# Kernel optimization log

Hardware: AMD Instinct MI355X
Metric: run time of the kernel (lower is better)

## Reference

```python
import jax, jax.numpy as jnp
import numpy as np
import math

B, S, D, H = 4, 1024, 512, 8
DK = D // H
NEG = -1e32


def setup_inputs() -> dict:
    key = jax.random.key(0)
    ks = jax.random.split(key, 16)
    f = lambda k, shape: jax.random.normal(k, shape, dtype=jnp.float32)
    w = 1.0 / math.sqrt(D)  # xavier-ish scale
    return {
        'query_mean': f(ks[0], (B, S, D)),
        'query_cov': f(ks[1], (B, S, D)),
        'key_mean': f(ks[2], (B, S, D)),
        'key_cov': f(ks[3], (B, S, D)),
        'values_mean': f(ks[4], (B, S, D)),
        'values_cov': f(ks[5], (B, S, D)),
        'Wk_mean': f(ks[6], (D, D)) * w, 'bk_mean': jnp.zeros((D,), jnp.float32),
        'Wk_cov': f(ks[7], (D, D)) * w, 'bk_cov': jnp.zeros((D,), jnp.float32),
        'Wv_mean': f(ks[8], (D, D)) * w, 'bv_mean': jnp.zeros((D,), jnp.float32),
        'Wv_cov': f(ks[9], (D, D)) * w, 'bv_cov': jnp.zeros((D,), jnp.float32),
        'Wo_mean': f(ks[10], (D, D)) * w, 'bo_mean': jnp.zeros((D,), jnp.float32),
        'Wo_cov': f(ks[11], (D, D)) * w, 'bo_cov': jnp.zeros((D,), jnp.float32),
        'gammas': f(ks[12], (H, 1, 1)) * 0.1,
        'mask': jnp.tril(jnp.ones((1, 1, S, S), dtype=jnp.int32)),
    }


def _forward(query_mean, query_cov, key_mean, key_cov, values_mean, values_cov,
             Wk_mean, bk_mean, Wk_cov, bk_cov, Wv_mean, bv_mean, Wv_cov, bv_cov,
             Wo_mean, bo_mean, Wo_cov, bo_cov, gammas, mask):
    def heads(x, W, b):  # [B,S,D] -> [B,H,S,DK]
        return (x @ W + b).reshape(B, S, H, DK).transpose(0, 2, 1, 3)

    # kq_same=True: queries and keys share the k linears
    qm = heads(query_mean, Wk_mean, bk_mean)
    qc = heads(query_cov, Wk_cov, bk_cov)
    km = heads(key_mean, Wk_mean, bk_mean)
    kc = heads(key_cov, Wk_cov, bk_cov)
    vm = heads(values_mean, Wv_mean, bv_mean)
    vc = heads(values_cov, Wv_cov, bv_cov)

    inv = 1.0 / math.sqrt(DK)
    sm = jnp.einsum('bhqd,bhkd->bhqk', qm, km) * inv  # [B,H,S,S]
    sc = jnp.einsum('bhqd,bhkd->bhqk', qc, kc) * inv

    maskf = mask.astype(jnp.float32)
    # position_effect[i,j] = |j - i|
    pos = jnp.abs(jnp.arange(S)[None, :] - jnp.arange(S)[:, None]).astype(jnp.float32)[None, None]

    def dist_scores(s):
        p = jax.nn.softmax(jnp.where(mask == 0, NEG, s), axis=-1) * maskf
        cum = jnp.cumsum(p, axis=-1)
        tot = jnp.sum(p, axis=-1, keepdims=True)
        return jnp.sqrt(jnp.clip((tot - cum) * pos, 0.0, None))

    dm = jax.lax.stop_gradient(dist_scores(sm))  # torch no_grad + detach
    dc = jax.lax.stop_gradient(dist_scores(sc))

    gv = -jax.nn.softplus(gammas)[None]  # [1,H,1,1]
    em = jnp.clip(jnp.exp(dm * gv), 1e-5, 1e5)
    ec = jnp.clip(jnp.exp(dc * gv), 1e-5, 1e5)

    am = jax.nn.softmax(jnp.where(mask == 0, NEG, sm * em), axis=-1)
    ac = jax.nn.softmax(jnp.where(mask == 0, NEG, sc * ec), axis=-1)

    om = jnp.einsum('bhqk,bhkd->bhqd', am, vm).transpose(0, 2, 1, 3).reshape(B, S, D)
    oc = jnp.einsum('bhqk,bhkd->bhqd', ac, vc).transpose(0, 2, 1, 3).reshape(B, S, D)
    return om @ Wo_mean + bo_mean, oc @ Wo_cov + bo_cov


def reference(query_mean, query_cov, key_mean, key_cov, values_mean, values_cov,
              Wk_mean, bk_mean, Wk_cov, bk_cov, Wv_mean, bv_mean, Wv_cov, bv_cov,
              Wo_mean, bo_mean, Wo_cov, bo_cov, gammas, mask):
    return _forward(query_mean, query_cov, key_mean, key_cov, values_mean, values_cov,
                    Wk_mean, bk_mean, Wk_cov, bk_cov, Wv_mean, bv_mean, Wv_cov, bv_cov,
                    Wo_mean, bo_mean, Wo_cov, bo_cov, gammas, mask)
```

## Files before the change

kernel.cpp:

```cpp
#include <hip/hip_runtime.h>
#include <hip/hip_bf16.h>
#include <math.h>

constexpr int B_  = 4;
constexpr int S_  = 1024;
constexpr int D_  = 512;
constexpr int H_  = 8;
constexpr int DK_ = 64;
constexpr int MROWS_ = B_ * S_;
constexpr size_t SZ_ = (size_t)B_ * H_ * S_ * DK_;
constexpr size_t WSZ_ = (size_t)D_ * D_;

typedef __attribute__((ext_vector_type(8))) short bf16x8;
typedef __attribute__((ext_vector_type(4))) float f32x4;

__device__ __forceinline__ float bf2f(unsigned short u) {
  union { unsigned int u; float f; } v; v.u = (unsigned int)u << 16; return v.f;
}
__device__ __forceinline__ unsigned short f2bf(float f) {
  union { float f; unsigned int u; } v; v.f = f;
  unsigned int r = v.u + 0x7FFFu + ((v.u >> 16) & 1u);
  return (unsigned short)(r >> 16);
}
__device__ __forceinline__ unsigned short f2bf_ru(float f) {
  union { float f; unsigned int u; } v; v.f = f;
  return (unsigned short)((v.u + 0x8000u) >> 16);
}

__device__ __forceinline__ float ex2(float x) {
#if __has_builtin(__builtin_amdgcn_exp2f)
  return __builtin_amdgcn_exp2f(x);
#else
  float r; asm("v_exp_f32 %0, %1" : "=v"(r) : "v"(x)); return r;
#endif
}
__device__ __forceinline__ float fsqrt_raw(float x) {
#if __has_builtin(__builtin_amdgcn_sqrtf)
  return __builtin_amdgcn_sqrtf(x);
#else
  float r; asm("v_sqrt_f32 %0, %1" : "=v"(r) : "v"(x)); return r;
#endif
}
__device__ __forceinline__ float frcp_raw(float x) {
#if __has_builtin(__builtin_amdgcn_rcpf)
  return __builtin_amdgcn_rcpf(x);
#else
  float r; asm("v_rcp_f32 %0, %1" : "=v"(r) : "v"(x)); return r;
#endif
}

template <int CTRL>
__device__ __forceinline__ float dpp_mov_f(float x) {
  return __builtin_bit_cast(float,
      __builtin_amdgcn_update_dpp(0, __builtin_bit_cast(int, x), CTRL, 0xF, 0xF, true));
}
__device__ __forceinline__ float scan16(float v) {
  v += dpp_mov_f<0x111>(v);
  v += dpp_mov_f<0x112>(v);
  v += dpp_mov_f<0x114>(v);
  v += dpp_mov_f<0x118>(v);
  return v;
}
__device__ __forceinline__ float red16(float v) {
  v += dpp_mov_f<0x128>(v);
  v += dpp_mov_f<0x124>(v);
  v += dpp_mov_f<0x122>(v);
  v += dpp_mov_f<0x121>(v);
  return v;
}
__device__ __forceinline__ float bcast15(float v) {
  return __builtin_bit_cast(float,
      __builtin_amdgcn_ds_swizzle(__builtin_bit_cast(int, v), 0x01F0));
}

__device__ __forceinline__ void gll16(const unsigned short* g, unsigned short* l) {
  __builtin_amdgcn_global_load_lds(
      (const __attribute__((address_space(1))) unsigned int*)g,
      (__attribute__((address_space(3))) unsigned int*)l, 16, 0, 0);
}

struct CvtArgs { const float* src[6]; unsigned short* dst; };

__global__ __launch_bounds__(256) void a2bf(CvtArgs a) {
  const int z = blockIdx.z;
  const float* __restrict__ src = a.src[z];
  unsigned short* __restrict__ dst = a.dst + (size_t)z * MROWS_ * D_;
  const int idx = blockIdx.x * 256 + threadIdx.x;
#pragma unroll
  for (int i = 0; i < 8; ++i) {
    const size_t j = (size_t)idx + (size_t)i * 65536;
    const float4 v = *(const float4*)&src[j * 4];
    ushort4 p;
    p.x = f2bf(v.x); p.y = f2bf(v.y); p.z = f2bf(v.z); p.w = f2bf(v.w);
    *(ushort4*)&dst[j * 4] = p;
  }
}

struct TpArgs { const float* W[6]; unsigned short* out[6]; };

__global__ __launch_bounds__(256) void wtrans(TpArgs a) {
  const int z = blockIdx.z;
  const float* __restrict__ W = a.W[z];
  unsigned short* __restrict__ out = a.out[z];
  __shared__ float T[64][65];
  const int tid = threadIdx.x;
  const int tx = blockIdx.x & 7, ty = blockIdx.x >> 3;
  const int k0 = ty * 64, n0 = tx * 64;
#pragma unroll
  for (int i = 0; i < 4; ++i) {
    const int idx = tid + i * 256;
    const int r = idx >> 4, c4 = (idx & 15) * 4;
    const float4 w = *(const float4*)&W[(size_t)(k0 + r) * D_ + n0 + c4];
    T[r][c4 + 0] = w.x; T[r][c4 + 1] = w.y; T[r][c4 + 2] = w.z; T[r][c4 + 3] = w.w;
  }
  __syncthreads();
#pragma unroll
  for (int i = 0; i < 4; ++i) {
    const int idx = tid + i * 256;
    const int n = idx >> 4, kc = (idx & 15) * 4;
    ushort4 pk;
    pk.x = f2bf(T[kc + 0][n]); pk.y = f2bf(T[kc + 1][n]);
    pk.z = f2bf(T[kc + 2][n]); pk.w = f2bf(T[kc + 3][n]);
    *(ushort4*)&out[(size_t)(n0 + n) * D_ + k0 + kc] = pk;
  }
}

struct ProjArgs {
  const unsigned short* A[6]; const unsigned short* Wt[6]; const float* bias[6];
  unsigned short* out[6]; int vmode[6];
};

__global__ __launch_bounds__(256) void proj_mfma(ProjArgs args) {
  const int z = blockIdx.z;
  const unsigned short* __restrict__ A = args.A[z];
  const unsigned short* __restrict__ Wt = args.Wt[z];
  const float* __restrict__ bias = args.bias[z];
  unsigned short* __restrict__ out = args.out[z];
  const int vmode = args.vmode[z];

  __shared__ unsigned short Abuf[128][32];
  __shared__ unsigned short Bbuf[128][32];
  const int tid = threadIdx.x, wv = tid >> 6, lane = tid & 63;
  const int quad = lane >> 4, l16 = lane & 15;
  const int wm = wv >> 1, wn = wv & 1;
  const int n0 = blockIdx.x * 128, m0 = blockIdx.y * 128;

  f32x4 acc[4][4];
#pragma unroll
  for (int i = 0; i < 4; ++i)
#pragma unroll
    for (int j = 0; j < 4; ++j) acc[i][j] = (f32x4){0.f, 0.f, 0.f, 0.f};

  for (int kt = 0; kt < 16; ++kt) {
    const int k0 = kt * 32;
    __syncthreads();
#pragma unroll
    for (int i = 0; i < 2; ++i) {
      const int idx = tid + i * 256;
      const int m = idx >> 2, c = idx & 3;
      gll16(&A[(size_t)(m0 + m) * D_ + k0 + c * 8], &Abuf[m][c * 8]);
    }
#pragma unroll
    for (int i = 0; i < 2; ++i) {
      const int idx = tid + i * 256;
      const int n = idx >> 2, c = idx & 3;
      gll16(&Wt[(size_t)(n0 + n) * D_ + k0 + c * 8], &Bbuf[n][c * 8]);
    }
    __syncthreads();

    bf16x8 af[4], bfr[4];
#pragma unroll
    for (int i = 0; i < 4; ++i) af[i] = *(const bf16x8*)&Abuf[wm * 64 + i * 16 + l16][quad * 8];
#pragma unroll
    for (int j = 0; j < 4; ++j) bfr[j] = *(const bf16x8*)&Bbuf[wn * 64 + j * 16 + l16][quad * 8];
#pragma unroll
    for (int i = 0; i < 4; ++i)
#pragma unroll
      for (int j = 0; j < 4; ++j)
        acc[i][j] = __builtin_amdgcn_mfma_f32_16x16x32_bf16(af[i], bfr[j], acc[i][j], 0, 0, 0);
  }

#pragma unroll
  for (int j = 0; j < 4; ++j) {
    const int col = n0 + wn * 64 + j * 16 + l16;
    const float bv = bias[col];
    const int h = col >> 6, dk = col & 63;
#pragma unroll
    for (int i = 0; i < 4; ++i) {
      const int mbase = m0 + wm * 64 + i * 16 + quad * 4;
      const int b = mbase >> 10;
      if (!vmode) {
#pragma unroll
        for (int r = 0; r < 4; ++r) {
          const int s = (mbase + r) & 1023;
          out[(((size_t)b * H_ + h) * S_ + s) * DK_ + dk] = f2bf(acc[i][j][r] + bv);
        }
      } else {
        const int s = mbase & 1023;
        ushort4 pk;
        pk.x = f2bf(acc[i][j][0] + bv); pk.y = f2bf(acc[i][j][1] + bv);
        pk.z = f2bf(acc[i][j][2] + bv); pk.w = f2bf(acc[i][j][3] + bv);
        *(ushort4*)&out[(((size_t)b * H_ + h) * DK_ + dk) * S_ + s] = pk;
      }
    }
  }
}

struct OutArgs {
  const unsigned short* A[2]; const unsigned short* Wt[2];
  const float* bias[2]; float* out[2];
};

__global__ __launch_bounds__(256) void out_mfma(OutArgs args) {
  const int z = blockIdx.z;
  const unsigned short* __restrict__ A = args.A[z];
  const unsigned short* __restrict__ Wt = args.Wt[z];
  const float* __restrict__ bias = args.bias[z];
  float* __restrict__ out = args.out[z];

  __shared__ unsigned short Abuf[128][32];
  __shared__ unsigned short Bbuf[128][32];
  const int tid = threadIdx.x, wv = tid >> 6, lane = tid & 63;
  const int quad = lane >> 4, l16 = lane & 15;
  const int wm = wv >> 1, wn = wv & 1;
  const int n0 = blockIdx.x * 128, m0 = blockIdx.y * 128;

  f32x4 acc[4][4];
#pragma unroll
  for (int i = 0; i < 4; ++i)
#pragma unroll
    for (int j = 0; j < 4; ++j) acc[i][j] = (f32x4){0.f, 0.f, 0.f, 0.f};

  for (int kt = 0; kt < 16; ++kt) {
    const int k0 = kt * 32;
    __syncthreads();
#pragma unroll
    for (int i = 0; i < 2; ++i) {
      const int idx = tid + i * 256;
      const int m = idx >> 2, c = idx & 3;
      gll16(&A[(size_t)(m0 + m) * D_ + k0 + c * 8], &Abuf[m][c * 8]);
    }
#pragma unroll
    for (int i = 0; i < 2; ++i) {
      const int idx = tid + i * 256;
      const int n = idx >> 2, c = idx & 3;
      gll16(&Wt[(size_t)(n0 + n) * D_ + k0 + c * 8], &Bbuf[n][c * 8]);
    }
    __syncthreads();

    bf16x8 af[4], bfr[4];
#pragma unroll
    for (int i = 0; i < 4; ++i) af[i] = *(const bf16x8*)&Abuf[wm * 64 + i * 16 + l16][quad * 8];
#pragma unroll
    for (int j = 0; j < 4; ++j) bfr[j] = *(const bf16x8*)&Bbuf[wn * 64 + j * 16 + l16][quad * 8];
#pragma unroll
    for (int i = 0; i < 4; ++i)
#pragma unroll
      for (int j = 0; j < 4; ++j)
        acc[i][j] = __builtin_amdgcn_mfma_f32_16x16x32_bf16(af[i], bfr[j], acc[i][j], 0, 0, 0);
  }

#pragma unroll
  for (int j = 0; j < 4; ++j) {
    const int col = n0 + wn * 64 + j * 16 + l16;
    const float bv = bias[col];
#pragma unroll
    for (int i = 0; i < 4; ++i) {
      const int mbase = m0 + wm * 64 + i * 16 + quad * 4;
#pragma unroll
      for (int r = 0; r < 4; ++r)
        out[(size_t)(mbase + r) * D_ + col] = acc[i][j][r] + bv;
    }
  }
}

__global__ __launch_bounds__(512) void attn_mfma(
    const unsigned short* __restrict__ qkv, const float* __restrict__ gammas,
    unsigned short* __restrict__ Obase)
{
  __shared__ unsigned short Ps[8][16][72];

  const int tid = threadIdx.x;
  const int w = tid >> 6, lane = tid & 63, quad = lane >> 4, l16 = lane & 15;
  const int bh = blockIdx.x;
  const int pair = blockIdx.y;
  const int ch = blockIdx.z;
  const int qt = (w < 4) ? (15 - pair) : pair;
  const int wq = w & 3;
  const int q0 = qt << 6;
  const int b = bh >> 3, h = bh & 7;

  constexpr float SC_ = 0.125f * 1.4426950408889634f;
  constexpr float LOG2E_ = 1.4426950408889634f;

  const unsigned short* Q  = qkv + (size_t)ch * 3 * SZ_ + (size_t)bh * S_ * DK_;
  const unsigned short* K  = qkv + (size_t)ch * 3 * SZ_ + SZ_ + (size_t)bh * S_ * DK_;
  const unsigned short* Vt = qkv + (size_t)ch * 3 * SZ_ + 2 * SZ_ + (size_t)bh * (size_t)DK_ * S_;
  unsigned short* O = Obase + (size_t)ch * SZ_;

  const float g = gammas[h];
  const float gv2 = -(fmaxf(g, 0.f) + log1pf(__expf(-fabsf(g)))) * LOG2E_;

  const unsigned short* Qrow = Q + (size_t)(q0 + wq * 16 + l16) * DK_;
  const bf16x8 qf0 = *(const bf16x8*)(Qrow + quad * 8);
  const bf16x8 qf1 = *(const bf16x8*)(Qrow + 32 + quad * 8);
  const int myrow = q0 + wq * 16 + quad * 4;

  float Tacc[4] = {0.f, 0.f, 0.f, 0.f};
  for (int kt = 0; kt <= qt; ++kt) {
    f32x4 sa[4];
#pragma unroll
    for (int cb = 0; cb < 4; ++cb) {
      const unsigned short* Kr = K + (size_t)(kt * 64 + cb * 16 + l16) * DK_;
      const bf16x8 kf0 = *(const bf16x8*)(Kr + quad * 8);
      const bf16x8 kf1 = *(const bf16x8*)(Kr + 32 + quad * 8);
      f32x4 a = {0.f, 0.f, 0.f, 0.f};
      a = __builtin_amdgcn_mfma_f32_16x16x32_bf16(qf0, kf0, a, 0, 0, 0);
      a = __builtin_amdgcn_mfma_f32_16x16x32_bf16(qf1, kf1, a, 0, 0, 0);
      sa[cb] = a;
    }
    if (kt == qt) {
#pragma unroll
      for (int cb = 0; cb < 4; ++cb)
#pragma unroll
        for (int r = 0; r < 4; ++r) {
          float e = ex2(sa[cb][r] * SC_);
          if ((kt * 64 + cb * 16 + l16) > (myrow + r)) e = 0.f;
          Tacc[r] += e;
        }
    } else {
#pragma unroll
      for (int cb = 0; cb < 4; ++cb)
#pragma unroll
        for (int r = 0; r < 4; ++r)
          Tacc[r] += ex2(sa[cb][r] * SC_);
    }
  }
  float invT[4];
#pragma unroll
  for (int r = 0; r < 4; ++r) invT[r] = frcp_raw(red16(Tacc[r]));

  float carry[4] = {0.f, 0.f, 0.f, 0.f};
  float l2a[4] = {0.f, 0.f, 0.f, 0.f};
  f32x4 oacc[4];
#pragma unroll
  for (int cb = 0; cb < 4; ++cb) oacc[cb] = (f32x4){0.f, 0.f, 0.f, 0.f};

  for (int kt = 0; kt <= qt; ++kt) {
    bf16x8 vf0[4], vf1[4];
#pragma unroll
    for (int cb = 0; cb < 4; ++cb) {
      const unsigned short* Vr = Vt + (size_t)(cb * 16 + l16) * S_ + kt * 64;
      vf0[cb] = *(const bf16x8*)(Vr + quad * 8);
      vf1[cb] = *(const bf16x8*)(Vr + 32 + quad * 8);
    }

    f32x4 sa[4];
#pragma unroll
    for (int cb = 0; cb < 4; ++cb) {
      const unsigned short* Kr = K + (size_t)(kt * 64 + cb * 16 + l16) * DK_;
      const bf16x8 kf0 = *(const bf16x8*)(Kr + quad * 8);
      const bf16x8 kf1 = *(const bf16x8*)(Kr + 32 + quad * 8);
      f32x4 a = {0.f, 0.f, 0.f, 0.f};
      a = __builtin_amdgcn_mfma_f32_16x16x32_bf16(qf0, kf0, a, 0, 0, 0);
      a = __builtin_amdgcn_mfma_f32_16x16x32_bf16(qf1, kf1, a, 0, 0, 0);
      sa[cb] = a;
    }
#pragma unroll
    for (int cb = 0; cb < 4; ++cb)
#pragma unroll
      for (int r = 0; r < 4; ++r) sa[cb][r] *= SC_;
    if (kt == qt) {
#pragma unroll
      for (int cb = 0; cb < 4; ++cb)
#pragma unroll
        for (int r = 0; r < 4; ++r)
          if ((kt * 64 + cb * 16 + l16) > (myrow + r)) sa[cb][r] = -1e30f;
    }

#pragma unroll
    for (int r = 0; r < 4; ++r) {
      float v0 = scan16(ex2(sa[0][r]));
      float v1 = scan16(ex2(sa[1][r]));
      float v2 = scan16(ex2(sa[2][r]));
      float v3 = scan16(ex2(sa[3][r]));
      const float tt0 = bcast15(v0), tt1 = bcast15(v1);
      const float tt2 = bcast15(v2), tt3 = bcast15(v3);
      const float base = carry[r];
      const float p01 = tt0 + tt1, p012 = p01 + tt2;
      const float cum0 = (base + v0) * invT[r];
      const float cum1 = (base + tt0 + v1) * invT[r];
      const float cum2 = (base + p01 + v2) * invT[r];
      const float cum3 = (base + p012 + v3) * invT[r];
      carry[r] = base + p012 + tt3;

      const float bpos = (float)(myrow + r) - (float)(kt * 64 + l16);
      float dd, st0, st1, st2, st3;
      dd = fsqrt_raw(fmaxf((1.f - cum0) * bpos, 0.f));
      st0 = sa[0][r] * fmaxf(ex2(dd * gv2), 1e-5f);
      dd = fsqrt_raw(fmaxf((1.f - cum1) * (bpos - 16.f), 0.f));
      st1 = sa[1][r] * fmaxf(ex2(dd * gv2), 1e-5f);
      dd = fsqrt_raw(fmaxf((1.f - cum2) * (bpos - 32.f), 0.f));
      st2 = sa[2][r] * fmaxf(ex2(dd * gv2), 1e-5f);
      dd = fsqrt_raw(fmaxf((1.f - cum3) * (bpos - 48.f), 0.f));
      st3 = sa[3][r] * fmaxf(ex2(dd * gv2), 1e-5f);

      const float w0 = ex2(st0), w1 = ex2(st1);
      const float w2 = ex2(st2), w3 = ex2(st3);
      l2a[r] += (w0 + w1) + (w2 + w3);
      const int prow = quad * 4 + r;
      Ps[w][prow][ 0 + l16] = f2bf_ru(w0);
      Ps[w][prow][16 + l16] = f2bf_ru(w1);
      Ps[w][prow][32 + l16] = f2bf_ru(w2);
      Ps[w][prow][48 + l16] = f2bf_ru(w3);
    }
    asm volatile("s_waitcnt lgkmcnt(0)" ::: "memory");

    const bf16x8 pf0 = *(const bf16x8*)&Ps[w][l16][quad * 8];
    const bf16x8 pf1 = *(const bf16x8*)&Ps[w][l16][32 + quad * 8];
#pragma unroll
    for (int cb = 0; cb < 4; ++cb) {
      oacc[cb] = __builtin_amdgcn_mfma_f32_16x16x32_bf16(pf0, vf0[cb], oacc[cb], 0, 0, 0);
      oacc[cb] = __builtin_amdgcn_mfma_f32_16x16x32_bf16(pf1, vf1[cb], oacc[cb], 0, 0, 0);
    }
  }

#pragma unroll
  for (int r = 0; r < 4; ++r) {
    const float inv = frcp_raw(red16(l2a[r]));
    const int srow = myrow + r;
    const size_t base = ((size_t)b * S_ + srow) * D_ + h * DK_;
    O[base +  0 + l16] = f2bf(oacc[0][r] * inv);
    O[base + 16 + l16] = f2bf(oacc[1][r] * inv);
    O[base + 32 + l16] = f2bf(oacc[2][r] * inv);
    O[base + 48 + l16] = f2bf(oacc[3][r] * inv);
  }
}

extern "C" void kernel_launch(void* const* d_in, const int* in_sizes, int n_in,
                              void* d_out, int out_size, void* d_ws, size_t ws_size,
                              hipStream_t stream) {
  const float* query_mean  = (const float*)d_in[0];
  const float* query_cov   = (const float*)d_in[1];
  const float* key_mean    = (const float*)d_in[2];
  const float* key_cov     = (const float*)d_in[3];
  const float* values_mean = (const float*)d_in[4];
  const float* values_cov  = (const float*)d_in[5];
  const float* Wk_mean = (const float*)d_in[6];
  const float* bk_mean = (const float*)d_in[7];
  const float* Wk_cov  = (const float*)d_in[8];
  const float* bk_cov  = (const float*)d_in[9];
  const float* Wv_mean = (const float*)d_in[10];
  const float* bv_mean = (const float*)d_in[11];
  const float* Wv_cov  = (const float*)d_in[12];
  const float* bv_cov  = (const float*)d_in[13];
  const float* Wo_mean = (const float*)d_in[14];
  const float* bo_mean = (const float*)d_in[15];
  const float* Wo_cov  = (const float*)d_in[16];
  const float* bo_cov  = (const float*)d_in[17];
  const float* gammas  = (const float*)d_in[18];

  unsigned short* qkv  = (unsigned short*)d_ws;
  unsigned short* obuf = qkv + 6 * SZ_;
  unsigned short* abf  = qkv + 8 * SZ_;
  unsigned short* Wot  = qkv + 14 * SZ_;
  unsigned short* Wt4  = (unsigned short*)d_out;
  float* out = (float*)d_out;

  TpArgs t1;
  t1.W[0] = Wk_mean; t1.W[1] = Wv_mean; t1.W[2] = Wk_cov; t1.W[3] = Wv_cov;
  t1.W[4] = Wo_mean; t1.W[5] = Wo_cov;
  for (int i = 0; i < 4; ++i) t1.out[i] = Wt4 + (size_t)i * WSZ_;
  t1.out[4] = Wot; t1.out[5] = Wot + WSZ_;
  wtrans<<<dim3(64, 1, 6), 256, 0, stream>>>(t1);

  CvtArgs cv;
  cv.src[0] = query_mean; cv.src[1] = key_mean; cv.src[2] = values_mean;
  cv.src[3] = query_cov;  cv.src[4] = key_cov;  cv.src[5] = values_cov;
  cv.dst = abf;
  a2bf<<<dim3(256, 1, 6), 256, 0, stream>>>(cv);

  ProjArgs pa;
  const int   wIdx[6] = {0, 0, 1, 2, 2, 3};
  const float* pb[6] = {bk_mean, bk_mean, bv_mean, bk_cov, bk_cov, bv_cov};
  const int pv[6] = {0, 0, 1, 0, 0, 1};
  for (int i = 0; i < 6; ++i) {
    pa.A[i] = abf + (size_t)i * MROWS_ * D_;
    pa.Wt[i] = Wt4 + (size_t)wIdx[i] * WSZ_; pa.bias[i] = pb[i];
    pa.out[i] = qkv + (size_t)i * SZ_; pa.vmode[i] = pv[i];
  }
  proj_mfma<<<dim3(4, 32, 6), 256, 0, stream>>>(pa);

  attn_mfma<<<dim3(32, 8, 2), 512, 0, stream>>>(qkv, gammas, obuf);

  OutArgs oa;
  oa.A[0] = obuf;        oa.A[1] = obuf + SZ_;
  oa.Wt[0] = Wot;        oa.Wt[1] = Wot + WSZ_;
  oa.bias[0] = bo_mean;  oa.bias[1] = bo_cov;
  oa.out[0] = out;       oa.out[1] = out + (size_t)MROWS_ * D_;
  out_mfma<<<dim3(4, 32, 2), 256, 0, stream>>>(oa);
}
```

Baseline: 265.0 us.

## Merge prep kernels and widen GEMM K-tile to 64 with XOR-swizzled LDS

Merges the weight-transpose and activation-to-bf16 conversion kernels into one launch. Most of the weight-transpose blocks (blockIdx.x >= 64) exit immediately, so some idle blocks are launched. The projection and output GEMMs now stage 64-wide K tiles in LDS, giving half as many sync rounds, and use an XOR swizzle on the 16-byte column chunks to avoid LDS bank conflicts on the fragment reads. The cost is double the LDS per block, which may lower occupancy.

Measured after the change: 268.1 us. Within noise of the previous version (+1.1%).

```diff
diff --git a/kernel.cpp b/kernel.cpp
--- a/kernel.cpp
+++ b/kernel.cpp
@@ -79,49 +79,50 @@
       (__attribute__((address_space(3))) unsigned int*)l, 16, 0, 0);
 }
 
-struct CvtArgs { const float* src[6]; unsigned short* dst; };
-
-__global__ __launch_bounds__(256) void a2bf(CvtArgs a) {
+struct PrepArgs {
+  const float* W[6]; unsigned short* wout[6];
+  const float* src[6]; unsigned short* adst;
+};
+
+__global__ __launch_bounds__(256) void prep(PrepArgs a) {
+  __shared__ float T[64][65];
   const int z = blockIdx.z;
-  const float* __restrict__ src = a.src[z];
-  unsigned short* __restrict__ dst = a.dst + (size_t)z * MROWS_ * D_;
-  const int idx = blockIdx.x * 256 + threadIdx.x;
-#pragma unroll
-  for (int i = 0; i < 8; ++i) {
-    const size_t j = (size_t)idx + (size_t)i * 65536;
-    const float4 v = *(const float4*)&src[j * 4];
-    ushort4 p;
-    p.x = f2bf(v.x); p.y = f2bf(v.y); p.z = f2bf(v.z); p.w = f2bf(v.w);
-    *(ushort4*)&dst[j * 4] = p;
-  }
-}
-
-struct TpArgs { const float* W[6]; unsigned short* out[6]; };
-
-__global__ __launch_bounds__(256) void wtrans(TpArgs a) {
-  const int z = blockIdx.z;
-  const float* __restrict__ W = a.W[z];
-  unsigned short* __restrict__ out = a.out[z];
-  __shared__ float T[64][65];
   const int tid = threadIdx.x;
-  const int tx = blockIdx.x & 7, ty = blockIdx.x >> 3;
-  const int k0 = ty * 64, n0 = tx * 64;
-#pragma unroll
-  for (int i = 0; i < 4; ++i) {
-    const int idx = tid + i * 256;
-    const int r = idx >> 4, c4 = (idx & 15) * 4;
-    const float4 w = *(const float4*)&W[(size_t)(k0 + r) * D_ + n0 + c4];
-    T[r][c4 + 0] = w.x; T[r][c4 + 1] = w.y; T[r][c4 + 2] = w.z; T[r][c4 + 3] = w.w;
-  }
-  __syncthreads();
-#pragma unroll
-  for (int i = 0; i < 4; ++i) {
-    const int idx = tid + i * 256;
-    const int n = idx >> 4, kc = (idx & 15) * 4;
-    ushort4 pk;
-    pk.x = f2bf(T[kc + 0][n]); pk.y = f2bf(T[kc + 1][n]);
-    pk.z = f2bf(T[kc + 2][n]); pk.w = f2bf(T[kc + 3][n]);
-    *(ushort4*)&out[(size_t)(n0 + n) * D_ + k0 + kc] = pk;
+  if (z < 6) {
+    if (blockIdx.x >= 64) return;
+    const float* __restrict__ W = a.W[z];
+    unsigned short* __restrict__ out = a.wout[z];
+    const int tx = blockIdx.x & 7, ty = blockIdx.x >> 3;
+    const int k0 = ty * 64, n0 = tx * 64;
+#pragma unroll
+    for (int i = 0; i < 4; ++i) {
+      const int idx = tid + i * 256;
+      const int r = idx >> 4, c4 = (idx & 15) * 4;
+      const float4 w = *(const float4*)&W[(size_t)(k0 + r) * D_ + n0 + c4];
+      T[r][c4 + 0] = w.x; T[r][c4 + 1] = w.y; T[r][c4 + 2] = w.z; T[r][c4 + 3] = w.w;
+    }
+    __syncthreads();
+#pragma unroll
+    for (int i = 0; i < 4; ++i) {
+      const int idx = tid + i * 256;
+      const int n = idx >> 4, kc = (idx & 15) * 4;
+      ushort4 pk;
+      pk.x = f2bf(T[kc + 0][n]); pk.y = f2bf(T[kc + 1][n]);
+      pk.z = f2bf(T[kc + 2][n]); pk.w = f2bf(T[kc + 3][n]);
+      *(ushort4*)&out[(size_t)(n0 + n) * D_ + k0 + kc] = pk;
+    }
+  } else {
+    const float* __restrict__ src = a.src[z - 6];
+    unsigned short* __restrict__ dst = a.adst + (size_t)(z - 6) * SZ_;
+    const int idx = blockIdx.x * 256 + tid;
+#pragma unroll
+    for (int i = 0; i < 8; ++i) {
+      const size_t j = (size_t)idx + (size_t)i * 65536;
+      const float4 v = *(const float4*)&src[j * 4];
+      ushort4 p;
+      p.x = f2bf(v.x); p.y = f2bf(v.y); p.z = f2bf(v.z); p.w = f2bf(v.w);
+      *(ushort4*)&dst[j * 4] = p;
+    }
   }
 }
 
@@ -138,8 +139,8 @@
   unsigned short* __restrict__ out = args.out[z];
   const int vmode = args.vmode[z];
 
-  __shared__ unsigned short Abuf[128][32];
-  __shared__ unsigned short Bbuf[128][32];
+  __shared__ unsigned short Abuf[128][64];
+  __shared__ unsigned short Bbuf[128][64];
   const int tid = threadIdx.x, wv = tid >> 6, lane = tid & 63;
   const int quad = lane >> 4, l16 = lane & 15;
   const int wm = wv >> 1, wn = wv & 1;
@@ -151,33 +152,42 @@
 #pragma unroll
     for (int j = 0; j < 4; ++j) acc[i][j] = (f32x4){0.f, 0.f, 0.f, 0.f};
 
-  for (int kt = 0; kt < 16; ++kt) {
-    const int k0 = kt * 32;
+  for (int kt = 0; kt < 8; ++kt) {
+    const int k0 = kt * 64;
     __syncthreads();
 #pragma unroll
-    for (int i = 0; i < 2; ++i) {
+    for (int i = 0; i < 4; ++i) {
       const int idx = tid + i * 256;
-      const int m = idx >> 2, c = idx & 3;
-      gll16(&A[(size_t)(m0 + m) * D_ + k0 + c * 8], &Abuf[m][c * 8]);
-    }
-#pragma unroll
-    for (int i = 0; i < 2; ++i) {
+      const int m = idx >> 3, c = idx & 7;
+      gll16(&A[(size_t)(m0 + m) * D_ + k0 + (c ^ (m & 7)) * 8], &Abuf[m][c * 8]);
+    }
+#pragma unroll
+    for (int i = 0; i < 4; ++i) {
       const int idx = tid + i * 256;
-      const int n = idx >> 2, c = idx & 3;
-      gll16(&Wt[(size_t)(n0 + n) * D_ + k0 + c * 8], &Bbuf[n][c * 8]);
+      const int n = idx >> 3, c = idx & 7;
+      gll16(&Wt[(size_t)(n0 + n) * D_ + k0 + (c ^ (n & 7)) * 8], &Bbuf[n][c * 8]);
     }
     __syncthreads();
 
-    bf16x8 af[4], bfr[4];
-#pragma unroll
-    for (int i = 0; i < 4; ++i) af[i] = *(const bf16x8*)&Abuf[wm * 64 + i * 16 + l16][quad * 8];
-#pragma unroll
-    for (int j = 0; j < 4; ++j) bfr[j] = *(const bf16x8*)&Bbuf[wn * 64 + j * 16 + l16][quad * 8];
-#pragma unroll
-    for (int i = 0; i < 4; ++i)
-#pragma unroll
-      for (int j = 0; j < 4; ++j)
-        acc[i][j] = __builtin_amdgcn_mfma_f32_16x16x32_bf16(af[i], bfr[j], acc[i][j], 0, 0, 0);
+#pragma unroll
+    for (int kk = 0; kk < 2; ++kk) {
+      bf16x8 af[4], bfr[4];
+#pragma unroll
+      for (int i = 0; i < 4; ++i) {
+        const int row = wm * 64 + i * 16 + l16;
+        af[i] = *(const bf16x8*)&Abuf[row][(((kk << 2) | quad) ^ (row & 7)) * 8];
+      }
+#pragma unroll
+      for (int j = 0; j < 4; ++j) {
+        const int row = wn * 64 + j * 16 + l16;
+        bfr[j] = *(const bf16x8*)&Bbuf[row][(((kk << 2) | quad) ^ (row & 7)) * 8];
+      }
+#pragma unroll
+      for (int i = 0; i < 4; ++i)
+#pragma unroll
+        for (int j = 0; j < 4; ++j)
+          acc[i][j] = __builtin_amdgcn_mfma_f32_16x16x32_bf16(af[i], bfr[j], acc[i][j], 0, 0, 0);
+    }
   }
 
 #pragma unroll
@@ -218,8 +228,8 @@
   const float* __restrict__ bias = args.bias[z];
   float* __restrict__ out = args.out[z];
 
-  __shared__ unsigned short Abuf[128][32];
-  __shared__ unsigned short Bbuf[128][32];
+  __shared__ unsigned short Abuf[128][64];
+  __shared__ unsigned short Bbuf[128][64];
   const int tid = threadIdx.x, wv = tid >> 6, lane = tid & 63;
   const int quad = lane >> 4, l16 = lane & 15;
   const int wm = wv >> 1, wn = wv & 1;
@@ -231,33 +241,42 @@
 #pragma unroll
     for (int j = 0; j < 4; ++j) acc[i][j] = (f32x4){0.f, 0.f, 0.f, 0.f};
 
-  for (int kt = 0; kt < 16; ++kt) {
-    const int k0 = kt * 32;
+  for (int kt = 0; kt < 8; ++kt) {
+    const int k0 = kt * 64;
     __syncthreads();
 #pragma unroll
-    for (int i = 0; i < 2; ++i) {
+    for (int i = 0; i < 4; ++i) {
       const int idx = tid + i * 256;
-      const int m = idx >> 2, c = idx & 3;
-      gll16(&A[(size_t)(m0 + m) * D_ + k0 + c * 8], &Abuf[m][c * 8]);
-    }
-#pragma unroll
-    for (int i = 0; i < 2; ++i) {
+      const int m = idx >> 3, c = idx & 7;
+      gll16(&A[(size_t)(m0 + m) * D_ + k0 + (c ^ (m & 7)) * 8], &Abuf[m][c * 8]);
+    }
+#pragma unroll
+    for (int i = 0; i < 4; ++i) {
       const int idx = tid + i * 256;
-      const int n = idx >> 2, c = idx & 3;
-      gll16(&Wt[(size_t)(n0 + n) * D_ + k0 + c * 8], &Bbuf[n][c * 8]);
+      const int n = idx >> 3, c = idx & 7;
+      gll16(&Wt[(size_t)(n0 + n) * D_ + k0 + (c ^ (n & 7)) * 8], &Bbuf[n][c * 8]);
     }
     __syncthreads();
 
-    bf16x8 af[4], bfr[4];
-#pragma unroll
-    for (int i = 0; i < 4; ++i) af[i] = *(const bf16x8*)&Abuf[wm * 64 + i * 16 + l16][quad * 8];
-#pragma unroll
-    for (int j = 0; j < 4; ++j) bfr[j] = *(const bf16x8*)&Bbuf[wn * 64 + j * 16 + l16][quad * 8];
-#pragma unroll
-    for (int i = 0; i < 4; ++i)
-#pragma unroll
-      for (int j = 0; j < 4; ++j)
-        acc[i][j] = __builtin_amdgcn_mfma_f32_16x16x32_bf16(af[i], bfr[j], acc[i][j], 0, 0, 0);
+#pragma unroll
+    for (int kk = 0; kk < 2; ++kk) {
+      bf16x8 af[4], bfr[4];
+#pragma unroll
+      for (int i = 0; i < 4; ++i) {
+        const int row = wm * 64 + i * 16 + l16;
+        af[i] = *(const bf16x8*)&Abuf[row][(((kk << 2) | quad) ^ (row & 7)) * 8];
+      }
+#pragma unroll
+      for (int j = 0; j < 4; ++j) {
+        const int row = wn * 64 + j * 16 + l16;
+        bfr[j] = *(const bf16x8*)&Bbuf[row][(((kk << 2) | quad) ^ (row & 7)) * 8];
+      }
+#pragma unroll
+      for (int i = 0; i < 4; ++i)
+#pragma unroll
+        for (int j = 0; j < 4; ++j)
+          acc[i][j] = __builtin_amdgcn_mfma_f32_16x16x32_bf16(af[i], bfr[j], acc[i][j], 0, 0, 0);
+    }
   }
 
 #pragma unroll
@@ -467,25 +486,22 @@
   unsigned short* Wt4  = (unsigned short*)d_out;
   float* out = (float*)d_out;
 
-  TpArgs t1;
-  t1.W[0] = Wk_mean; t1.W[1] = Wv_mean; t1.W[2] = Wk_cov; t1.W[3] = Wv_cov;
-  t1.W[4] = Wo_mean; t1.W[5] = Wo_cov;
-  for (int i = 0; i < 4; ++i) t1.out[i] = Wt4 + (size_t)i * WSZ_;
-  t1.out[4] = Wot; t1.out[5] = Wot + WSZ_;
-  wtrans<<<dim3(64, 1, 6), 256, 0, stream>>>(t1);
-
-  CvtArgs cv;
-  cv.src[0] = query_mean; cv.src[1] = key_mean; cv.src[2] = values_mean;
-  cv.src[3] = query_cov;  cv.src[4] = key_cov;  cv.src[5] = values_cov;
-  cv.dst = abf;
-  a2bf<<<dim3(256, 1, 6), 256, 0, stream>>>(cv);
+  PrepArgs pr;
+  pr.W[0] = Wk_mean; pr.W[1] = Wv_mean; pr.W[2] = Wk_cov; pr.W[3] = Wv_cov;
+  pr.W[4] = Wo_mean; pr.W[5] = Wo_cov;
+  for (int i = 0; i < 4; ++i) pr.wout[i] = Wt4 + (size_t)i * WSZ_;
+  pr.wout[4] = Wot; pr.wout[5] = Wot + WSZ_;
+  pr.src[0] = query_mean; pr.src[1] = key_mean; pr.src[2] = values_mean;
+  pr.src[3] = query_cov;  pr.src[4] = key_cov;  pr.src[5] = values_cov;
+  pr.adst = abf;
+  prep<<<dim3(256, 1, 12), 256, 0, stream>>>(pr);
 
   ProjArgs pa;
   const int   wIdx[6] = {0, 0, 1, 2, 2, 3};
   const float* pb[6] = {bk_mean, bk_mean, bv_mean, bk_cov, bk_cov, bv_cov};
   const int pv[6] = {0, 0, 1, 0, 0, 1};
   for (int i = 0; i < 6; ++i) {
-    pa.A[i] = abf + (size_t)i * MROWS_ * D_;
+    pa.A[i] = abf + (size_t)i * SZ_;
     pa.Wt[i] = Wt4 + (size_t)wIdx[i] * WSZ_; pa.bias[i] = pb[i];
     pa.out[i] = qkv + (size_t)i * SZ_; pa.vmode[i] = pv[i];
   }
```
